# Performance work log

Measured on AMD Instinct MI355X. Metric: run time of the kernel, lower is better.

Reference implementation:

```python
import jax, jax.numpy as jnp
import numpy as np

N = 100000
E = 600000
D_IN = 128
D_HID = 128
D_OUT = 16


def _glorot(key, shape):
    fan_in, fan_out = shape[1], shape[0]
    lim = np.sqrt(6.0 / (fan_in + fan_out))
    return jax.random.uniform(key, shape, jnp.float32, -lim, lim)


def setup_inputs() -> dict:
    key = jax.random.key(0)
    ks = jax.random.split(key, 8)
    x = jax.random.normal(ks[0], (N, D_IN), jnp.float32)
    edge_index = jax.random.randint(ks[1], (2, E), 0, N, jnp.int32)
    dims = [(D_IN, D_HID), (D_HID, D_HID), (D_HID, D_OUT)]
    params = {}
    for i, (din, dout) in enumerate(dims):
        params[f"Wl{i}"] = _glorot(jax.random.fold_in(ks[2], i), (dout, din))  # lin_l (aggregated neighbors)
        params[f"bl{i}"] = jnp.zeros((dout,), jnp.float32)
        params[f"Wr{i}"] = _glorot(jax.random.fold_in(ks[3], i), (dout, din))  # lin_r (root/self)
    return {"x": x, "edge_index": edge_index, **params}


def _sage_conv(x, src, dst, Wl, bl, Wr):
    # mean aggregation of source features at target nodes
    msgs = x[src]                                              # [E, d] gather
    agg = jax.ops.segment_sum(msgs, dst, num_segments=N)       # [N, d]
    cnt = jax.ops.segment_sum(jnp.ones((src.shape[0],), x.dtype), dst, num_segments=N)
    mean = agg / jnp.maximum(cnt, 1.0)[:, None]
    return mean @ Wl.T + bl + x @ Wr.T


def reference(x, edge_index, Wl0, bl0, Wr0, Wl1, bl1, Wr1, Wl2, bl2, Wr2):
    src, dst = edge_index[0], edge_index[1]
    h = jax.nn.relu(_sage_conv(x, src, dst, Wl0, bl0, Wr0))  # dropout is identity in eval mode
    h = jax.nn.relu(_sage_conv(h, src, dst, Wl1, bl1, Wr1))
    h = _sage_conv(h, src, dst, Wl2, bl2, Wr2)
    return jax.nn.log_softmax(h, axis=1)
```

## Files before the change

### kernel.cpp

```cpp
#include <hip/hip_runtime.h>
#include <math.h>

#define NN 100000
#define NE 600000
#define DD 128
#define NB_SCAN 98

#define NB_CAST 12500
#define NB_PREPW 64
#define NB_PREPW2 8
#define NB_DEG 2344

typedef __attribute__((ext_vector_type(8))) short bf16x8;
typedef __attribute__((ext_vector_type(4))) float f32x4;
typedef unsigned short u16;
typedef unsigned int u32;

__device__ __forceinline__ float bflo(u32 w) {
    union { u32 i; float f; } v; v.i = w << 16; return v.f;
}
__device__ __forceinline__ float bfhi(u32 w) {
    union { u32 i; float f; } v; v.i = w & 0xffff0000u; return v.f;
}
__device__ __forceinline__ u16 f2bf(float f) {
    union { float f; u32 u; } v; v.f = f;
    u32 r = v.u + 0x7fffu + ((v.u >> 16) & 1u);
    return (u16)(r >> 16);
}


__global__ __launch_bounds__(256) void k_setup(const float* __restrict__ x,
                                               u16* __restrict__ xb,
                                               const float* __restrict__ Wl0,
                                               const float* __restrict__ Wr0,
                                               const float* __restrict__ Wl1,
                                               const float* __restrict__ Wr1,
                                               const float* __restrict__ Wl2,
                                               const float* __restrict__ Wr2,
                                               u16* __restrict__ Wc0,
                                               u16* __restrict__ Wc1,
                                               u16* __restrict__ Wc2,
                                               const int* __restrict__ dst,
                                               int* __restrict__ deg,
                                               u16* __restrict__ H1,
                                               u16* __restrict__ hl2b) {
    int b = blockIdx.x;
    int tid = threadIdx.x;
    if (b < NB_CAST) {
        int i = b * 256 + tid;
        float4 v = reinterpret_cast<const float4*>(x)[i];
        ushort4 o;
        o.x = f2bf(v.x); o.y = f2bf(v.y); o.z = f2bf(v.z); o.w = f2bf(v.w);
        reinterpret_cast<ushort4*>(xb)[i] = o;
    } else if (b < NB_CAST + NB_PREPW) {
        int t = (b - NB_CAST) * 256 + tid;
        int j = t >> 7, k = t & 127;
        Wc0[j * 256 + k]       = f2bf(Wl0[t]);
        Wc0[j * 256 + 128 + k] = f2bf(Wr0[t]);
        Wc1[j * 256 + k]       = f2bf(Wl1[t]);
        Wc1[j * 256 + 128 + k] = f2bf(Wr1[t]);
    } else if (b < NB_CAST + NB_PREPW + NB_PREPW2) {
        int t = (b - NB_CAST - NB_PREPW) * 256 + tid;
        int j = t >> 7, k = t & 127;
        Wc2[j * 128 + k]        = f2bf(Wl2[t]);
        Wc2[(16 + j) * 128 + k] = f2bf(Wr2[t]);
    } else if (b < NB_CAST + NB_PREPW + NB_PREPW2 + NB_DEG) {
        int e = (b - NB_CAST - NB_PREPW - NB_PREPW2) * 256 + tid;
        if (e < NE) atomicAdd(&deg[dst[e]], 1);
    } else {
        if (tid < DD) { xb[(size_t)NN * DD + tid] = 0; H1[(size_t)NN * DD + tid] = 0; }
        if (tid < 16) hl2b[(size_t)NN * 16 + tid] = 0;
    }
}


__global__ __launch_bounds__(256) void k_scan1(const int* __restrict__ deg,
                                               int* __restrict__ bsum,
                                               int* __restrict__ hist) {
    __shared__ int sm[256];
    __shared__ int lh[32];
    int t = threadIdx.x;
    if (t < 32) lh[t] = 0;
    int idx = blockIdx.x * 1024 + t * 4;
    int4 v = make_int4(0, 0, 0, 0);
    if (idx + 3 < NN) v = *reinterpret_cast<const int4*>(deg + idx);
    else {
        if (idx     < NN) v.x = deg[idx];
        if (idx + 1 < NN) v.y = deg[idx + 1];
        if (idx + 2 < NN) v.z = deg[idx + 2];
        if (idx + 3 < NN) v.w = deg[idx + 3];
    }
    int p0 = (v.x + 7) & ~7, p1 = (v.y + 7) & ~7, p2 = (v.z + 7) & ~7, p3 = (v.w + 7) & ~7;
    sm[t] = p0 + p1 + p2 + p3;
    __syncthreads();
    if (idx     < NN) atomicAdd(&lh[min(p0 >> 3, 31)], 1);
    if (idx + 1 < NN) atomicAdd(&lh[min(p1 >> 3, 31)], 1);
    if (idx + 2 < NN) atomicAdd(&lh[min(p2 >> 3, 31)], 1);
    if (idx + 3 < NN) atomicAdd(&lh[min(p3 >> 3, 31)], 1);
    __syncthreads();
    if (t < 32) atomicAdd(&hist[t], lh[t]);
    for (int off = 128; off > 0; off >>= 1) {
        if (t < off) sm[t] += sm[t + off];
        __syncthreads();
    }
    if (t == 0) bsum[blockIdx.x] = sm[0];
}

__global__ __launch_bounds__(128) void k_scan2(int* __restrict__ bsum,
                                               const int* __restrict__ hist,
                                               int* __restrict__ cursor) {
    __shared__ int sm[128];
    int t = threadIdx.x;
    int v = (t < NB_SCAN) ? bsum[t] : 0;
    sm[t] = v;
    __syncthreads();
    for (int off = 1; off < 128; off <<= 1) {
        int add = (t >= off) ? sm[t - off] : 0;
        __syncthreads();
        sm[t] += add;
        __syncthreads();
    }
    if (t < NB_SCAN) bsum[t] = (t == 0) ? 0 : sm[t - 1];
    if (t == 0) {
        int r = 0;
        for (int c = 31; c >= 0; --c) { cursor[c] = r; r += hist[c]; }
    }
}

__global__ __launch_bounds__(256) void k_scan3(const int* __restrict__ deg,
                                               const int* __restrict__ boff,
                                               int* __restrict__ cur,
                                               int* __restrict__ col2,
                                               int* __restrict__ cursor,
                                               int4* __restrict__ desc) {
    __shared__ int sm[256];
    __shared__ int lh[32];
    __shared__ int lb[32];
    int t = threadIdx.x;
    if (t < 32) lh[t] = 0;
    int idx = blockIdx.x * 1024 + t * 4;
    int4 v = make_int4(0, 0, 0, 0);
    if (idx + 3 < NN) v = *reinterpret_cast<const int4*>(deg + idx);
    else {
        if (idx     < NN) v.x = deg[idx];
        if (idx + 1 < NN) v.y = deg[idx + 1];
        if (idx + 2 < NN) v.z = deg[idx + 2];
        if (idx + 3 < NN) v.w = deg[idx + 3];
    }
    int p0 = (v.x + 7) & ~7, p1 = (v.y + 7) & ~7, p2 = (v.z + 7) & ~7, p3 = (v.w + 7) & ~7;
    sm[t] = p0 + p1 + p2 + p3;
    __syncthreads();
    for (int off = 1; off < 256; off <<= 1) {
        int add = (t >= off) ? sm[t - off] : 0;
        __syncthreads();
        sm[t] += add;
        __syncthreads();
    }
    int run = boff[blockIdx.x] + ((t == 0) ? 0 : sm[t - 1]);
    int d[4] = {v.x, v.y, v.z, v.w};
    int p[4] = {p0, p1, p2, p3};
    int begs[4], ci[4], myi[4];
#pragma unroll
    for (int i = 0; i < 4; ++i) {
        if (idx + i < NN) {
            begs[i] = run;
            cur[idx + i] = run;
            for (int q = run + d[i]; q < run + p[i]; ++q) col2[q] = NN;
            ci[i] = min(p[i] >> 3, 31);
            myi[i] = atomicAdd(&lh[ci[i]], 1);
            run += p[i];
        }
    }
    __syncthreads();
    if (t < 32 && lh[t] > 0) lb[t] = atomicAdd(&cursor[t], lh[t]);
    __syncthreads();
#pragma unroll
    for (int i = 0; i < 4; ++i) {
        if (idx + i < NN) {
            float iv = 1.0f / (float)(d[i] > 0 ? d[i] : 1);
            desc[lb[ci[i]] + myi[i]] =
                make_int4(idx + i, begs[i], begs[i] + p[i], __float_as_int(iv));
        }
    }
}

__global__ __launch_bounds__(256) void k_scatter(const int* __restrict__ src,
                                                 const int* __restrict__ dst,
                                                 int* __restrict__ cur,
                                                 int* __restrict__ col2) {
    int e = blockIdx.x * 256 + threadIdx.x;
    if (e < NE) {
        int p = atomicAdd(&cur[dst[e]], 1);
        col2[p] = src[e];
    }
}


__global__ __launch_bounds__(256) void k_fused_layer(const u16* __restrict__ X,
                                                     const int* __restrict__ col2,
                                                     const int4* __restrict__ desc,
                                                     const u16* __restrict__ Wc,
                                                     const float* __restrict__ b,
                                                     u16* __restrict__ out) {
    __shared__ u16 XK[16 * 256];
    char* lds = reinterpret_cast<char*>(XK);

    int tid = threadIdx.x;
    int nl = tid >> 4;
    int sl = tid & 15;
    int4 d = desc[blockIdx.x * 16 + nl];
    int n = d.x, beg = d.y, end = d.z;
    float iv = __int_as_float(d.w);

    uint4 xv = *reinterpret_cast<const uint4*>(X + (size_t)n * DD + sl * 8);
    *reinterpret_cast<uint4*>(lds + nl * 512 + ((256 + sl * 16) ^ ((nl & 7) << 4))) = xv;

    float a0 = 0.f, a1 = 0.f, a2 = 0.f, a3 = 0.f, a4 = 0.f, a5 = 0.f, a6 = 0.f, a7 = 0.f;
    for (int e = beg; e < end; e += 8) {
        int4 c0 = *reinterpret_cast<const int4*>(col2 + e);
        int4 c1 = *reinterpret_cast<const int4*>(col2 + e + 4);
        uint4 v0 = *reinterpret_cast<const uint4*>(X + (size_t)c0.x * DD + sl * 8);
        uint4 v1 = *reinterpret_cast<const uint4*>(X + (size_t)c0.y * DD + sl * 8);
        uint4 v2 = *reinterpret_cast<const uint4*>(X + (size_t)c0.z * DD + sl * 8);
        uint4 v3 = *reinterpret_cast<const uint4*>(X + (size_t)c0.w * DD + sl * 8);
        uint4 v4 = *reinterpret_cast<const uint4*>(X + (size_t)c1.x * DD + sl * 8);
        uint4 v5 = *reinterpret_cast<const uint4*>(X + (size_t)c1.y * DD + sl * 8);
        uint4 v6 = *reinterpret_cast<const uint4*>(X + (size_t)c1.z * DD + sl * 8);
        uint4 v7 = *reinterpret_cast<const uint4*>(X + (size_t)c1.w * DD + sl * 8);
        a0 += ((bflo(v0.x) + bflo(v1.x)) + (bflo(v2.x) + bflo(v3.x)))
            + ((bflo(v4.x) + bflo(v5.x)) + (bflo(v6.x) + bflo(v7.x)));
        a1 += ((bfhi(v0.x) + bfhi(v1.x)) + (bfhi(v2.x) + bfhi(v3.x)))
            + ((bfhi(v4.x) + bfhi(v5.x)) + (bfhi(v6.x) + bfhi(v7.x)));
        a2 += ((bflo(v0.y) + bflo(v1.y)) + (bflo(v2.y) + bflo(v3.y)))
            + ((bflo(v4.y) + bflo(v5.y)) + (bflo(v6.y) + bflo(v7.y)));
        a3 += ((bfhi(v0.y) + bfhi(v1.y)) + (bfhi(v2.y) + bfhi(v3.y)))
            + ((bfhi(v4.y) + bfhi(v5.y)) + (bfhi(v6.y) + bfhi(v7.y)));
        a4 += ((bflo(v0.z) + bflo(v1.z)) + (bflo(v2.z) + bflo(v3.z)))
            + ((bflo(v4.z) + bflo(v5.z)) + (bflo(v6.z) + bflo(v7.z)));
        a5 += ((bfhi(v0.z) + bfhi(v1.z)) + (bfhi(v2.z) + bfhi(v3.z)))
            + ((bfhi(v4.z) + bfhi(v5.z)) + (bfhi(v6.z) + bfhi(v7.z)));
        a6 += ((bflo(v0.w) + bflo(v1.w)) + (bflo(v2.w) + bflo(v3.w)))
            + ((bflo(v4.w) + bflo(v5.w)) + (bflo(v6.w) + bflo(v7.w)));
        a7 += ((bfhi(v0.w) + bfhi(v1.w)) + (bfhi(v2.w) + bfhi(v3.w)))
            + ((bfhi(v4.w) + bfhi(v5.w)) + (bfhi(v6.w) + bfhi(v7.w)));
    }
    uint4 o;
    o.x = (u32)f2bf(a0 * iv) | ((u32)f2bf(a1 * iv) << 16);
    o.y = (u32)f2bf(a2 * iv) | ((u32)f2bf(a3 * iv) << 16);
    o.z = (u32)f2bf(a4 * iv) | ((u32)f2bf(a5 * iv) << 16);
    o.w = (u32)f2bf(a6 * iv) | ((u32)f2bf(a7 * iv) << 16);
    *reinterpret_cast<uint4*>(lds + nl * 512 + ((sl * 16) ^ ((nl & 7) << 4))) = o;
    __syncthreads();

    int wid = tid >> 6, lane = tid & 63;
    int cl = lane & 15, rq = lane >> 4;

    f32x4 acc0 = (f32x4){0.f, 0.f, 0.f, 0.f};
    f32x4 acc1 = (f32x4){0.f, 0.f, 0.f, 0.f};
    const u16* wbase = Wc + (size_t)(wid * 32 + cl) * 256 + rq * 8;
    const char* xbase = lds + cl * 512;
    int xmask = (cl & 7) << 4;
#pragma unroll
    for (int ks = 0; ks < 8; ++ks) {
        bf16x8 xf = *reinterpret_cast<const bf16x8*>(xbase + ((ks * 64 + rq * 16) ^ xmask));
        bf16x8 w0 = *reinterpret_cast<const bf16x8*>(wbase + ks * 32);
        bf16x8 w1 = *reinterpret_cast<const bf16x8*>(wbase + 16 * 256 + ks * 32);
        acc0 = __builtin_amdgcn_mfma_f32_16x16x32_bf16(w0, xf, acc0, 0, 0, 0);
        acc1 = __builtin_amdgcn_mfma_f32_16x16x32_bf16(w1, xf, acc1, 0, 0, 0);
    }
    __syncthreads();

#pragma unroll
    for (int jf = 0; jf < 2; ++jf) {
        f32x4 a = jf ? acc1 : acc0;
        int j0 = wid * 32 + jf * 16 + rq * 4;
        float4 bias = *reinterpret_cast<const float4*>(b + j0);
        float o0 = fmaxf(a[0] + bias.x, 0.f);
        float o1 = fmaxf(a[1] + bias.y, 0.f);
        float o2 = fmaxf(a[2] + bias.z, 0.f);
        float o3 = fmaxf(a[3] + bias.w, 0.f);
        uint2 pk;
        pk.x = (u32)f2bf(o0) | ((u32)f2bf(o1) << 16);
        pk.y = (u32)f2bf(o2) | ((u32)f2bf(o3) << 16);
        *reinterpret_cast<uint2*>(lds + cl * 512 + ((j0 * 2) ^ ((cl & 7) << 4))) = pk;
    }
    __syncthreads();

    uint4 ov = *reinterpret_cast<const uint4*>(lds + nl * 512 + ((sl * 16) ^ ((nl & 7) << 4)));
    *reinterpret_cast<uint4*>(out + (size_t)n * DD + sl * 8) = ov;
}


__global__ __launch_bounds__(256) void k_l2t(const u16* __restrict__ H,
                                             const u16* __restrict__ Wc2,
                                             u16* __restrict__ hl2b,
                                             float* __restrict__ hr2) {
    __shared__ u16 HS[32 * 128];
    char* lds = reinterpret_cast<char*>(HS);
    int tid = threadIdx.x;
    int r0 = tid >> 4, c0 = tid & 15;
#pragma unroll
    for (int p = 0; p < 2; ++p) {
        int r = p * 16 + r0;
        uint4 v = *reinterpret_cast<const uint4*>(H + (size_t)(blockIdx.x * 32 + r) * DD + c0 * 8);
        *reinterpret_cast<uint4*>(lds + r * 256 + ((c0 * 16) ^ ((r & 7) << 4))) = v;
    }
    __syncthreads();

    int wid = tid >> 6, lane = tid & 63, cl = lane & 15, rq = lane >> 4;
    int h = wid >> 1, jf = wid & 1;
    f32x4 acc = (f32x4){0.f, 0.f, 0.f, 0.f};
    const u16* wb = Wc2 + (size_t)(jf * 16 + cl) * 128 + rq * 8;
    int row = h * 16 + cl;
    const char* xb2 = lds + row * 256;
    int xm = (row & 7) << 4;
#pragma unroll
    for (int ks = 0; ks < 4; ++ks) {
        bf16x8 xf = *reinterpret_cast<const bf16x8*>(xb2 + ((ks * 64 + rq * 16) ^ xm));
        bf16x8 wf = *reinterpret_cast<const bf16x8*>(wb + ks * 32);
        acc = __builtin_amdgcn_mfma_f32_16x16x32_bf16(wf, xf, acc, 0, 0, 0);
    }
    int n = blockIdx.x * 32 + h * 16 + cl;
    if (jf == 0) {
        uint2 pk;
        pk.x = (u32)f2bf(acc[0]) | ((u32)f2bf(acc[1]) << 16);
        pk.y = (u32)f2bf(acc[2]) | ((u32)f2bf(acc[3]) << 16);
        *reinterpret_cast<uint2*>(hl2b + (size_t)n * 16 + rq * 4) = pk;
    } else {
        *reinterpret_cast<float4*>(hr2 + (size_t)n * 16 + rq * 4) =
            make_float4(acc[0], acc[1], acc[2], acc[3]);
    }
}

__global__ __launch_bounds__(256) void k_l2_final(const u16* __restrict__ hl2b,
                                                  const float* __restrict__ hr2,
                                                  const int* __restrict__ col2,
                                                  const int4* __restrict__ desc,
                                                  const float* __restrict__ b2,
                                                  float* __restrict__ out) {
    int tid = threadIdx.x;
    int ns = tid >> 3;
    int l  = tid & 7;
    int4 d = desc[blockIdx.x * 32 + ns];
    int n = d.x, beg = d.y, end = d.z;
    float iv = __int_as_float(d.w);

    float ag[16];
#pragma unroll
    for (int j = 0; j < 16; ++j) ag[j] = 0.f;
    for (int e = beg + l; e < end; e += 8) {
        const u16* r = hl2b + (size_t)col2[e] * 16;
        uint4 h0 = *reinterpret_cast<const uint4*>(r);
        uint4 h1 = *reinterpret_cast<const uint4*>(r + 8);
        ag[0] += bflo(h0.x); ag[1] += bfhi(h0.x); ag[2]  += bflo(h0.y); ag[3]  += bfhi(h0.y);
        ag[4] += bflo(h0.z); ag[5] += bfhi(h0.z); ag[6]  += bflo(h0.w); ag[7]  += bfhi(h0.w);
        ag[8] += bflo(h1.x); ag[9] += bfhi(h1.x); ag[10] += bflo(h1.y); ag[11] += bfhi(h1.y);
        ag[12] += bflo(h1.z); ag[13] += bfhi(h1.z); ag[14] += bflo(h1.w); ag[15] += bfhi(h1.w);
    }
#pragma unroll
    for (int m = 1; m <= 4; m <<= 1) {
#pragma unroll
        for (int j = 0; j < 16; ++j) ag[j] += __shfl_xor(ag[j], m);
    }
    if (l < 4) {
        float4 hr = *reinterpret_cast<const float4*>(hr2 + (size_t)n * 16 + l * 4);
        float4 bb = *reinterpret_cast<const float4*>(b2 + l * 4);
        float v0 = hr.x + bb.x + ag[l * 4 + 0] * iv;
        float v1 = hr.y + bb.y + ag[l * 4 + 1] * iv;
        float v2 = hr.z + bb.z + ag[l * 4 + 2] * iv;
        float v3 = hr.w + bb.w + ag[l * 4 + 3] * iv;
        float m4 = fmaxf(fmaxf(v0, v1), fmaxf(v2, v3));
        m4 = fmaxf(m4, __shfl_xor(m4, 1));
        m4 = fmaxf(m4, __shfl_xor(m4, 2));
        float s4 = expf(v0 - m4) + expf(v1 - m4) + expf(v2 - m4) + expf(v3 - m4);
        s4 += __shfl_xor(s4, 1);
        s4 += __shfl_xor(s4, 2);
        float lse = m4 + logf(s4);
        *reinterpret_cast<float4*>(out + (size_t)n * 16 + l * 4) =
            make_float4(v0 - lse, v1 - lse, v2 - lse, v3 - lse);
    }
}


extern "C" void kernel_launch(void* const* d_in, const int* in_sizes, int n_in,
                              void* d_out, int out_size, void* d_ws, size_t ws_size,
                              hipStream_t stream) {
    const float* x   = (const float*)d_in[0];
    const int*   ei  = (const int*)d_in[1];
    const float* Wl0 = (const float*)d_in[2];
    const float* bl0 = (const float*)d_in[3];
    const float* Wr0 = (const float*)d_in[4];
    const float* Wl1 = (const float*)d_in[5];
    const float* bl1 = (const float*)d_in[6];
    const float* Wr1 = (const float*)d_in[7];
    const float* Wl2 = (const float*)d_in[8];
    const float* bl2 = (const float*)d_in[9];
    const float* Wr2 = (const float*)d_in[10];
    float* out = (float*)d_out;

    const int* e_src = ei;
    const int* e_dst = ei + NE;

    char* ws = (char*)d_ws;
    size_t off = 0;
    auto carve = [&](size_t bytes) -> void* {
        void* p = ws + off;
        off = (off + bytes + 255) & ~(size_t)255;
        return p;
    };
    int*   deg  = (int*)carve((size_t)(NN + 128) * 4);
    int*   hist = deg + NN;
    int*   curs = deg + NN + 32;
    int*   cur  = (int*)carve((size_t)NN * 4);
    int*   bsum = (int*)carve(512 * 4);
    int*   col2 = (int*)carve((size_t)(NE + 7 * NN + 64) * 4);
    int4*  desc = (int4*)carve((size_t)NN * 16);
    u16*   xb   = (u16*)carve((size_t)(NN + 1) * DD * 2);
    u16*   H1   = (u16*)carve((size_t)(NN + 1) * DD * 2);
    u16*   H2   = (u16*)carve((size_t)NN * DD * 2);
    u16*   Wc0  = (u16*)carve((size_t)128 * 256 * 2);
    u16*   Wc1  = (u16*)carve((size_t)128 * 256 * 2);
    u16*   Wc2  = (u16*)carve((size_t)32 * 128 * 2);
    u16*   hl2b = (u16*)carve((size_t)(NN + 1) * 16 * 2);
    float* hr2  = (float*)carve((size_t)NN * 16 * 4);
    (void)ws_size; (void)in_sizes; (void)n_in; (void)out_size;

    hipMemsetAsync(deg, 0, (size_t)(NN + 128) * 4, stream);
    k_setup<<<NB_CAST + NB_PREPW + NB_PREPW2 + NB_DEG + 1, 256, 0, stream>>>(
        x, xb, Wl0, Wr0, Wl1, Wr1, Wl2, Wr2, Wc0, Wc1, Wc2, e_dst, deg, H1, hl2b);

    k_scan1<<<NB_SCAN, 256, 0, stream>>>(deg, bsum, hist);
    k_scan2<<<1, 128, 0, stream>>>(bsum, hist, curs);
    k_scan3<<<NB_SCAN, 256, 0, stream>>>(deg, bsum, cur, col2, curs, desc);
    k_scatter<<<(NE + 255) / 256, 256, 0, stream>>>(e_src, e_dst, cur, col2);

    k_fused_layer<<<NN / 16, 256, 0, stream>>>(xb, col2, desc, Wc0, bl0, H1);
    k_fused_layer<<<NN / 16, 256, 0, stream>>>(H1, col2, desc, Wc1, bl1, H2);

    k_l2t<<<NN / 32, 256, 0, stream>>>(H2, Wc2, hl2b, hr2);
    k_l2_final<<<NN / 32, 256, 0, stream>>>(hl2b, hr2, col2, desc, bl2, out);
}
```

Before: 240.4 us.

## Fuse layer-2 transform into layer-1 kernel, pad neighbor lists to 4, 32 nodes/block

The layer-1 fused kernel now also computes the final layer's two 16-wide projections from LDS, so the H2 intermediate and the k_l2t launch are gone. Each block now handles 32 nodes, with 8 lanes per node and 16 features per lane, and reuses each weight fragment across two MFMA node tiles. Neighbor lists are padded to multiples of 4 instead of 8, which cuts the dummy gathers on low-degree nodes. In exchange the kernel uses more LDS and registers per block, and the gather loop issues 4 neighbors per iteration with two 16-byte loads each.

```diff
diff --git a/kernel.cpp b/kernel.cpp
--- a/kernel.cpp
+++ b/kernel.cpp
@@ -90,13 +90,13 @@
         if (idx + 2 < NN) v.z = deg[idx + 2];
         if (idx + 3 < NN) v.w = deg[idx + 3];
     }
-    int p0 = (v.x + 7) & ~7, p1 = (v.y + 7) & ~7, p2 = (v.z + 7) & ~7, p3 = (v.w + 7) & ~7;
+    int p0 = (v.x + 3) & ~3, p1 = (v.y + 3) & ~3, p2 = (v.z + 3) & ~3, p3 = (v.w + 3) & ~3;
     sm[t] = p0 + p1 + p2 + p3;
     __syncthreads();
-    if (idx     < NN) atomicAdd(&lh[min(p0 >> 3, 31)], 1);
-    if (idx + 1 < NN) atomicAdd(&lh[min(p1 >> 3, 31)], 1);
-    if (idx + 2 < NN) atomicAdd(&lh[min(p2 >> 3, 31)], 1);
-    if (idx + 3 < NN) atomicAdd(&lh[min(p3 >> 3, 31)], 1);
+    if (idx     < NN) atomicAdd(&lh[min(p0 >> 2, 31)], 1);
+    if (idx + 1 < NN) atomicAdd(&lh[min(p1 >> 2, 31)], 1);
+    if (idx + 2 < NN) atomicAdd(&lh[min(p2 >> 2, 31)], 1);
+    if (idx + 3 < NN) atomicAdd(&lh[min(p3 >> 2, 31)], 1);
     __syncthreads();
     if (t < 32) atomicAdd(&hist[t], lh[t]);
     for (int off = 128; off > 0; off >>= 1) {
@@ -147,7 +147,7 @@
         if (idx + 2 < NN) v.z = deg[idx + 2];
         if (idx + 3 < NN) v.w = deg[idx + 3];
     }
-    int p0 = (v.x + 7) & ~7, p1 = (v.y + 7) & ~7, p2 = (v.z + 7) & ~7, p3 = (v.w + 7) & ~7;
+    int p0 = (v.x + 3) & ~3, p1 = (v.y + 3) & ~3, p2 = (v.z + 3) & ~3, p3 = (v.w + 3) & ~3;
     sm[t] = p0 + p1 + p2 + p3;
     __syncthreads();
     for (int off = 1; off < 256; off <<= 1) {
@@ -166,7 +166,7 @@
             begs[i] = run;
             cur[idx + i] = run;
             for (int q = run + d[i]; q < run + p[i]; ++q) col2[q] = NN;
-            ci[i] = min(p[i] >> 3, 31);
+            ci[i] = min(p[i] >> 2, 31);
             myi[i] = atomicAdd(&lh[ci[i]], 1);
             run += p[i];
         }
@@ -196,141 +196,159 @@
 }
 
 
+template<bool STORE, bool DOW2>
 __global__ __launch_bounds__(256) void k_fused_layer(const u16* __restrict__ X,
                                                      const int* __restrict__ col2,
                                                      const int4* __restrict__ desc,
                                                      const u16* __restrict__ Wc,
                                                      const float* __restrict__ b,
-                                                     u16* __restrict__ out) {
-    __shared__ u16 XK[16 * 256];
+                                                     u16* __restrict__ out,
+                                                     const u16* __restrict__ Wc2,
+                                                     u16* __restrict__ hl2b,
+                                                     float* __restrict__ hr2) {
+    __shared__ u16 XK[32 * 256];
     char* lds = reinterpret_cast<char*>(XK);
 
     int tid = threadIdx.x;
-    int nl = tid >> 4;
-    int sl = tid & 15;
-    int4 d = desc[blockIdx.x * 16 + nl];
+    int nl = tid >> 3;
+    int sl = tid & 7;
+    int4 d = desc[blockIdx.x * 32 + nl];
     int n = d.x, beg = d.y, end = d.z;
     float iv = __int_as_float(d.w);
-
-    uint4 xv = *reinterpret_cast<const uint4*>(X + (size_t)n * DD + sl * 8);
-    *reinterpret_cast<uint4*>(lds + nl * 512 + ((256 + sl * 16) ^ ((nl & 7) << 4))) = xv;
+    int m = (nl & 7) << 4;
+
+    {
+        const u16* xs = X + (size_t)n * DD + sl * 16;
+        uint4 s0 = *reinterpret_cast<const uint4*>(xs);
+        uint4 s1 = *reinterpret_cast<const uint4*>(xs + 8);
+        int boff = 256 + sl * 32;
+        *reinterpret_cast<uint4*>(lds + nl * 512 + (boff ^ m)) = s0;
+        *reinterpret_cast<uint4*>(lds + nl * 512 + ((boff + 16) ^ m)) = s1;
+    }
 
     float a0 = 0.f, a1 = 0.f, a2 = 0.f, a3 = 0.f, a4 = 0.f, a5 = 0.f, a6 = 0.f, a7 = 0.f;
-    for (int e = beg; e < end; e += 8) {
-        int4 c0 = *reinterpret_cast<const int4*>(col2 + e);
-        int4 c1 = *reinterpret_cast<const int4*>(col2 + e + 4);
-        uint4 v0 = *reinterpret_cast<const uint4*>(X + (size_t)c0.x * DD + sl * 8);
-        uint4 v1 = *reinterpret_cast<const uint4*>(X + (size_t)c0.y * DD + sl * 8);
-        uint4 v2 = *reinterpret_cast<const uint4*>(X + (size_t)c0.z * DD + sl * 8);
-        uint4 v3 = *reinterpret_cast<const uint4*>(X + (size_t)c0.w * DD + sl * 8);
-        uint4 v4 = *reinterpret_cast<const uint4*>(X + (size_t)c1.x * DD + sl * 8);
-        uint4 v5 = *reinterpret_cast<const uint4*>(X + (size_t)c1.y * DD + sl * 8);
-        uint4 v6 = *reinterpret_cast<const uint4*>(X + (size_t)c1.z * DD + sl * 8);
-        uint4 v7 = *reinterpret_cast<const uint4*>(X + (size_t)c1.w * DD + sl * 8);
-        a0 += ((bflo(v0.x) + bflo(v1.x)) + (bflo(v2.x) + bflo(v3.x)))
-            + ((bflo(v4.x) + bflo(v5.x)) + (bflo(v6.x) + bflo(v7.x)));
-        a1 += ((bfhi(v0.x) + bfhi(v1.x)) + (bfhi(v2.x) + bfhi(v3.x)))
-            + ((bfhi(v4.x) + bfhi(v5.x)) + (bfhi(v6.x) + bfhi(v7.x)));
-        a2 += ((bflo(v0.y) + bflo(v1.y)) + (bflo(v2.y) + bflo(v3.y)))
-            + ((bflo(v4.y) + bflo(v5.y)) + (bflo(v6.y) + bflo(v7.y)));
-        a3 += ((bfhi(v0.y) + bfhi(v1.y)) + (bfhi(v2.y) + bfhi(v3.y)))
-            + ((bfhi(v4.y) + bfhi(v5.y)) + (bfhi(v6.y) + bfhi(v7.y)));
-        a4 += ((bflo(v0.z) + bflo(v1.z)) + (bflo(v2.z) + bflo(v3.z)))
-            + ((bflo(v4.z) + bflo(v5.z)) + (bflo(v6.z) + bflo(v7.z)));
-        a5 += ((bfhi(v0.z) + bfhi(v1.z)) + (bfhi(v2.z) + bfhi(v3.z)))
-            + ((bfhi(v4.z) + bfhi(v5.z)) + (bfhi(v6.z) + bfhi(v7.z)));
-        a6 += ((bflo(v0.w) + bflo(v1.w)) + (bflo(v2.w) + bflo(v3.w)))
-            + ((bflo(v4.w) + bflo(v5.w)) + (bflo(v6.w) + bflo(v7.w)));
-        a7 += ((bfhi(v0.w) + bfhi(v1.w)) + (bfhi(v2.w) + bfhi(v3.w)))
-            + ((bfhi(v4.w) + bfhi(v5.w)) + (bfhi(v6.w) + bfhi(v7.w)));
-    }
-    uint4 o;
-    o.x = (u32)f2bf(a0 * iv) | ((u32)f2bf(a1 * iv) << 16);
-    o.y = (u32)f2bf(a2 * iv) | ((u32)f2bf(a3 * iv) << 16);
-    o.z = (u32)f2bf(a4 * iv) | ((u32)f2bf(a5 * iv) << 16);
-    o.w = (u32)f2bf(a6 * iv) | ((u32)f2bf(a7 * iv) << 16);
-    *reinterpret_cast<uint4*>(lds + nl * 512 + ((sl * 16) ^ ((nl & 7) << 4))) = o;
+    float a8 = 0.f, a9 = 0.f, a10 = 0.f, a11 = 0.f, a12 = 0.f, a13 = 0.f, a14 = 0.f, a15 = 0.f;
+    for (int e = beg; e < end; e += 4) {
+        int4 c = *reinterpret_cast<const int4*>(col2 + e);
+        const u16* p0 = X + (size_t)c.x * DD + sl * 16;
+        const u16* p1 = X + (size_t)c.y * DD + sl * 16;
+        const u16* p2 = X + (size_t)c.z * DD + sl * 16;
+        const u16* p3 = X + (size_t)c.w * DD + sl * 16;
+        uint4 v0 = *reinterpret_cast<const uint4*>(p0);
+        uint4 w0 = *reinterpret_cast<const uint4*>(p0 + 8);
+        uint4 v1 = *reinterpret_cast<const uint4*>(p1);
+        uint4 w1 = *reinterpret_cast<const uint4*>(p1 + 8);
+        uint4 v2 = *reinterpret_cast<const uint4*>(p2);
+        uint4 w2 = *reinterpret_cast<const uint4*>(p2 + 8);
+        uint4 v3 = *reinterpret_cast<const uint4*>(p3);
+        uint4 w3 = *reinterpret_cast<const uint4*>(p3 + 8);
+        a0  += (bflo(v0.x) + bflo(v1.x)) + (bflo(v2.x) + bflo(v3.x));
+        a1  += (bfhi(v0.x) + bfhi(v1.x)) + (bfhi(v2.x) + bfhi(v3.x));
+        a2  += (bflo(v0.y) + bflo(v1.y)) + (bflo(v2.y) + bflo(v3.y));
+        a3  += (bfhi(v0.y) + bfhi(v1.y)) + (bfhi(v2.y) + bfhi(v3.y));
+        a4  += (bflo(v0.z) + bflo(v1.z)) + (bflo(v2.z) + bflo(v3.z));
+        a5  += (bfhi(v0.z) + bfhi(v1.z)) + (bfhi(v2.z) + bfhi(v3.z));
+        a6  += (bflo(v0.w) + bflo(v1.w)) + (bflo(v2.w) + bflo(v3.w));
+        a7  += (bfhi(v0.w) + bfhi(v1.w)) + (bfhi(v2.w) + bfhi(v3.w));
+        a8  += (bflo(w0.x) + bflo(w1.x)) + (bflo(w2.x) + bflo(w3.x));
+        a9  += (bfhi(w0.x) + bfhi(w1.x)) + (bfhi(w2.x) + bfhi(w3.x));
+        a10 += (bflo(w0.y) + bflo(w1.y)) + (bflo(w2.y) + bflo(w3.y));
+        a11 += (bfhi(w0.y) + bfhi(w1.y)) + (bfhi(w2.y) + bfhi(w3.y));
+        a12 += (bflo(w0.z) + bflo(w1.z)) + (bflo(w2.z) + bflo(w3.z));
+        a13 += (bfhi(w0.z) + bfhi(w1.z)) + (bfhi(w2.z) + bfhi(w3.z));
+        a14 += (bflo(w0.w) + bflo(w1.w)) + (bflo(w2.w) + bflo(w3.w));
+        a15 += (bfhi(w0.w) + bfhi(w1.w)) + (bfhi(w2.w) + bfhi(w3.w));
+    }
+    uint4 o0, o1;
+    o0.x = (u32)f2bf(a0 * iv)  | ((u32)f2bf(a1 * iv)  << 16);
+    o0.y = (u32)f2bf(a2 * iv)  | ((u32)f2bf(a3 * iv)  << 16);
+    o0.z = (u32)f2bf(a4 * iv)  | ((u32)f2bf(a5 * iv)  << 16);
+    o0.w = (u32)f2bf(a6 * iv)  | ((u32)f2bf(a7 * iv)  << 16);
+    o1.x = (u32)f2bf(a8 * iv)  | ((u32)f2bf(a9 * iv)  << 16);
+    o1.y = (u32)f2bf(a10 * iv) | ((u32)f2bf(a11 * iv) << 16);
+    o1.z = (u32)f2bf(a12 * iv) | ((u32)f2bf(a13 * iv) << 16);
+    o1.w = (u32)f2bf(a14 * iv) | ((u32)f2bf(a15 * iv) << 16);
+    *reinterpret_cast<uint4*>(lds + nl * 512 + ((sl * 32) ^ m)) = o0;
+    *reinterpret_cast<uint4*>(lds + nl * 512 + ((sl * 32 + 16) ^ m)) = o1;
     __syncthreads();
 
     int wid = tid >> 6, lane = tid & 63;
     int cl = lane & 15, rq = lane >> 4;
-
-    f32x4 acc0 = (f32x4){0.f, 0.f, 0.f, 0.f};
-    f32x4 acc1 = (f32x4){0.f, 0.f, 0.f, 0.f};
+    int xm = (cl & 7) << 4;
+
+    f32x4 acc00 = (f32x4){0.f, 0.f, 0.f, 0.f};
+    f32x4 acc01 = (f32x4){0.f, 0.f, 0.f, 0.f};
+    f32x4 acc10 = (f32x4){0.f, 0.f, 0.f, 0.f};
+    f32x4 acc11 = (f32x4){0.f, 0.f, 0.f, 0.f};
     const u16* wbase = Wc + (size_t)(wid * 32 + cl) * 256 + rq * 8;
-    const char* xbase = lds + cl * 512;
-    int xmask = (cl & 7) << 4;
+    const char* x0b = lds + cl * 512;
+    const char* x1b = lds + (16 + cl) * 512;
 #pragma unroll
     for (int ks = 0; ks < 8; ++ks) {
-        bf16x8 xf = *reinterpret_cast<const bf16x8*>(xbase + ((ks * 64 + rq * 16) ^ xmask));
-        bf16x8 w0 = *reinterpret_cast<const bf16x8*>(wbase + ks * 32);
-        bf16x8 w1 = *reinterpret_cast<const bf16x8*>(wbase + 16 * 256 + ks * 32);
-        acc0 = __builtin_amdgcn_mfma_f32_16x16x32_bf16(w0, xf, acc0, 0, 0, 0);
-        acc1 = __builtin_amdgcn_mfma_f32_16x16x32_bf16(w1, xf, acc1, 0, 0, 0);
-    }
-    __syncthreads();
-
-#pragma unroll
-    for (int jf = 0; jf < 2; ++jf) {
-        f32x4 a = jf ? acc1 : acc0;
-        int j0 = wid * 32 + jf * 16 + rq * 4;
-        float4 bias = *reinterpret_cast<const float4*>(b + j0);
-        float o0 = fmaxf(a[0] + bias.x, 0.f);
-        float o1 = fmaxf(a[1] + bias.y, 0.f);
-        float o2 = fmaxf(a[2] + bias.z, 0.f);
-        float o3 = fmaxf(a[3] + bias.w, 0.f);
-        uint2 pk;
-        pk.x = (u32)f2bf(o0) | ((u32)f2bf(o1) << 16);
-        pk.y = (u32)f2bf(o2) | ((u32)f2bf(o3) << 16);
-        *reinterpret_cast<uint2*>(lds + cl * 512 + ((j0 * 2) ^ ((cl & 7) << 4))) = pk;
-    }
-    __syncthreads();
-
-    uint4 ov = *reinterpret_cast<const uint4*>(lds + nl * 512 + ((sl * 16) ^ ((nl & 7) << 4)));
-    *reinterpret_cast<uint4*>(out + (size_t)n * DD + sl * 8) = ov;
-}
-
-
-__global__ __launch_bounds__(256) void k_l2t(const u16* __restrict__ H,
-                                             const u16* __restrict__ Wc2,
-                                             u16* __restrict__ hl2b,
-                                             float* __restrict__ hr2) {
-    __shared__ u16 HS[32 * 128];
-    char* lds = reinterpret_cast<char*>(HS);
-    int tid = threadIdx.x;
-    int r0 = tid >> 4, c0 = tid & 15;
-#pragma unroll
-    for (int p = 0; p < 2; ++p) {
-        int r = p * 16 + r0;
-        uint4 v = *reinterpret_cast<const uint4*>(H + (size_t)(blockIdx.x * 32 + r) * DD + c0 * 8);
-        *reinterpret_cast<uint4*>(lds + r * 256 + ((c0 * 16) ^ ((r & 7) << 4))) = v;
-    }
-    __syncthreads();
-
-    int wid = tid >> 6, lane = tid & 63, cl = lane & 15, rq = lane >> 4;
-    int h = wid >> 1, jf = wid & 1;
-    f32x4 acc = (f32x4){0.f, 0.f, 0.f, 0.f};
-    const u16* wb = Wc2 + (size_t)(jf * 16 + cl) * 128 + rq * 8;
-    int row = h * 16 + cl;
-    const char* xb2 = lds + row * 256;
-    int xm = (row & 7) << 4;
-#pragma unroll
-    for (int ks = 0; ks < 4; ++ks) {
-        bf16x8 xf = *reinterpret_cast<const bf16x8*>(xb2 + ((ks * 64 + rq * 16) ^ xm));
-        bf16x8 wf = *reinterpret_cast<const bf16x8*>(wb + ks * 32);
-        acc = __builtin_amdgcn_mfma_f32_16x16x32_bf16(wf, xf, acc, 0, 0, 0);
-    }
-    int n = blockIdx.x * 32 + h * 16 + cl;
-    if (jf == 0) {
-        uint2 pk;
-        pk.x = (u32)f2bf(acc[0]) | ((u32)f2bf(acc[1]) << 16);
-        pk.y = (u32)f2bf(acc[2]) | ((u32)f2bf(acc[3]) << 16);
-        *reinterpret_cast<uint2*>(hl2b + (size_t)n * 16 + rq * 4) = pk;
-    } else {
-        *reinterpret_cast<float4*>(hr2 + (size_t)n * 16 + rq * 4) =
-            make_float4(acc[0], acc[1], acc[2], acc[3]);
-    }
-}
+        int xo = (ks * 64 + rq * 16) ^ xm;
+        bf16x8 xf0 = *reinterpret_cast<const bf16x8*>(x0b + xo);
+        bf16x8 xf1 = *reinterpret_cast<const bf16x8*>(x1b + xo);
+        bf16x8 wf0 = *reinterpret_cast<const bf16x8*>(wbase + ks * 32);
+        bf16x8 wf1 = *reinterpret_cast<const bf16x8*>(wbase + 16 * 256 + ks * 32);
+        acc00 = __builtin_amdgcn_mfma_f32_16x16x32_bf16(wf0, xf0, acc00, 0, 0, 0);
+        acc01 = __builtin_amdgcn_mfma_f32_16x16x32_bf16(wf1, xf0, acc01, 0, 0, 0);
+        acc10 = __builtin_amdgcn_mfma_f32_16x16x32_bf16(wf0, xf1, acc10, 0, 0, 0);
+        acc11 = __builtin_amdgcn_mfma_f32_16x16x32_bf16(wf1, xf1, acc11, 0, 0, 0);
+    }
+    __syncthreads();
+
+#pragma unroll
+    for (int g = 0; g < 2; ++g) {
+#pragma unroll
+        for (int jf = 0; jf < 2; ++jf) {
+            f32x4 a = g ? (jf ? acc11 : acc10) : (jf ? acc01 : acc00);
+            int j0 = wid * 32 + jf * 16 + rq * 4;
+            float4 bias = *reinterpret_cast<const float4*>(b + j0);
+            float o0f = fmaxf(a[0] + bias.x, 0.f);
+            float o1f = fmaxf(a[1] + bias.y, 0.f);
+            float o2f = fmaxf(a[2] + bias.z, 0.f);
+            float o3f = fmaxf(a[3] + bias.w, 0.f);
+            uint2 pk;
+            pk.x = (u32)f2bf(o0f) | ((u32)f2bf(o1f) << 16);
+            pk.y = (u32)f2bf(o2f) | ((u32)f2bf(o3f) << 16);
+            int row = g * 16 + cl;
+            *reinterpret_cast<uint2*>(lds + row * 512 + ((j0 * 2) ^ ((cl & 7) << 4))) = pk;
+        }
+    }
+    __syncthreads();
+
+    if (STORE) {
+        uint4 q0 = *reinterpret_cast<const uint4*>(lds + nl * 512 + ((sl * 32) ^ m));
+        uint4 q1 = *reinterpret_cast<const uint4*>(lds + nl * 512 + ((sl * 32 + 16) ^ m));
+        u16* orow = out + (size_t)n * DD + sl * 16;
+        *reinterpret_cast<uint4*>(orow) = q0;
+        *reinterpret_cast<uint4*>(orow + 8) = q1;
+    }
+
+    if (DOW2) {
+        int g = wid >> 1, tbl = wid & 1;
+        f32x4 a2 = (f32x4){0.f, 0.f, 0.f, 0.f};
+        const u16* wb = Wc2 + (size_t)(tbl * 16 + cl) * 128 + rq * 8;
+        const char* xb = lds + (size_t)(g * 16 + cl) * 512;
+#pragma unroll
+        for (int ks = 0; ks < 4; ++ks) {
+            bf16x8 xf = *reinterpret_cast<const bf16x8*>(xb + ((ks * 64 + rq * 16) ^ xm));
+            bf16x8 wf = *reinterpret_cast<const bf16x8*>(wb + ks * 32);
+            a2 = __builtin_amdgcn_mfma_f32_16x16x32_bf16(wf, xf, a2, 0, 0, 0);
+        }
+        int n2 = desc[blockIdx.x * 32 + g * 16 + cl].x;
+        if (tbl == 0) {
+            uint2 pk;
+            pk.x = (u32)f2bf(a2[0]) | ((u32)f2bf(a2[1]) << 16);
+            pk.y = (u32)f2bf(a2[2]) | ((u32)f2bf(a2[3]) << 16);
+            *reinterpret_cast<uint2*>(hl2b + (size_t)n2 * 16 + rq * 4) = pk;
+        } else {
+            *reinterpret_cast<float4*>(hr2 + (size_t)n2 * 16 + rq * 4) =
+                make_float4(a2[0], a2[1], a2[2], a2[3]);
+        }
+    }
+}
+
 
 __global__ __launch_bounds__(256) void k_l2_final(const u16* __restrict__ hl2b,
                                                   const float* __restrict__ hr2,
@@ -413,11 +431,10 @@
     int*   curs = deg + NN + 32;
     int*   cur  = (int*)carve((size_t)NN * 4);
     int*   bsum = (int*)carve(512 * 4);
-    int*   col2 = (int*)carve((size_t)(NE + 7 * NN + 64) * 4);
+    int*   col2 = (int*)carve((size_t)(NE + 3 * NN + 64) * 4);
     int4*  desc = (int4*)carve((size_t)NN * 16);
     u16*   xb   = (u16*)carve((size_t)(NN + 1) * DD * 2);
     u16*   H1   = (u16*)carve((size_t)(NN + 1) * DD * 2);
-    u16*   H2   = (u16*)carve((size_t)NN * DD * 2);
     u16*   Wc0  = (u16*)carve((size_t)128 * 256 * 2);
     u16*   Wc1  = (u16*)carve((size_t)128 * 256 * 2);
     u16*   Wc2  = (u16*)carve((size_t)32 * 128 * 2);
@@ -434,9 +451,11 @@
     k_scan3<<<NB_SCAN, 256, 0, stream>>>(deg, bsum, cur, col2, curs, desc);
     k_scatter<<<(NE + 255) / 256, 256, 0, stream>>>(e_src, e_dst, cur, col2);
 
-    k_fused_layer<<<NN / 16, 256, 0, stream>>>(xb, col2, desc, Wc0, bl0, H1);
-    k_fused_layer<<<NN / 16, 256, 0, stream>>>(H1, col2, desc, Wc1, bl1, H2);
-
-    k_l2t<<<NN / 32, 256, 0, stream>>>(H2, Wc2, hl2b, hr2);
+    k_fused_layer<true, false><<<NN / 32, 256, 0, stream>>>(
+        xb, col2, desc, Wc0, bl0, H1, nullptr, nullptr, nullptr);
+
+    k_fused_layer<false, true><<<NN / 32, 256, 0, stream>>>(
+        H1, col2, desc, Wc1, bl1, nullptr, Wc2, hl2b, hr2);
+
     k_l2_final<<<NN / 32, 256, 0, stream>>>(hl2b, hr2, col2, desc, bl2, out);
 }
```

Result: faster. 203.1 us (-15.5%).
